# Performance work log

Hardware: AMD Instinct MI355X
Metric: run time of the kernel (lower is better)

The kernel has to match this reference:

```python
import jax, jax.numpy as jnp
import numpy as np

H = 1024      # hidden_size
NH = 16       # num_heads
HD = H // NH  # head_dim


def setup_inputs() -> dict:
    key = jax.random.key(0)
    k1, k2, k3 = jax.random.split(key, 3)
    x = jax.random.normal(k1, (2, 2048, H), dtype=jnp.float32)
    # torch Linear weights: [out, in]; init ~ small scale
    w_qkv = jax.random.normal(k2, (3 * H, H), dtype=jnp.float32) * (1.0 / np.sqrt(H))
    w_out = jax.random.normal(k3, (H, H), dtype=jnp.float32) * (1.0 / np.sqrt(H))
    return {"x": x, "w_qkv": w_qkv, "w_out": w_out}


def reference(x, w_qkv, w_out):
    B, S, _ = x.shape
    qkv = jnp.einsum("bsh,oh->bso", x, w_qkv)              # [B,S,3H]
    qkv = qkv.reshape(B, S, 3, NH, HD).transpose(2, 0, 3, 1, 4)  # [3,B,NH,S,HD]
    q, k, v = qkv[0], qkv[1], qkv[2]
    scale = 1.0 / np.sqrt(HD)
    scores = jnp.einsum("bhqd,bhkd->bhqk", q, k) * scale   # [B,NH,S,S]
    causal = jnp.tril(jnp.ones((S, S), dtype=bool))
    scores = jnp.where(causal, scores, jnp.finfo(scores.dtype).min)
    attn = jax.nn.softmax(scores, axis=-1)
    out = jnp.einsum("bhqk,bhkd->bhqd", attn, v)           # [B,NH,S,HD]
    out = out.transpose(0, 2, 1, 3).reshape(B, S, H)
    return jnp.einsum("bsh,oh->bso", out, w_out)
```

## Files before the change

kernel.cpp:

```cpp
#include <hip/hip_runtime.h>
#include <hip/hip_fp16.h>


typedef _Float16 half8 __attribute__((ext_vector_type(8)));
typedef _Float16 half4 __attribute__((ext_vector_type(4)));
typedef float f32x4 __attribute__((ext_vector_type(4)));

typedef const __attribute__((address_space(1))) void gvoid_t;
typedef __attribute__((address_space(3))) void lvoid_t;

#define LOG2E 1.4426950408889634f
#define QSCALE (0.125f * LOG2E)

__global__ void cast_all_f16(const float* __restrict__ x, const float* __restrict__ wq,
                             const float* __restrict__ wo, _Float16* __restrict__ xh,
                             _Float16* __restrict__ wqh, _Float16* __restrict__ woh) {
  int i = blockIdx.x * blockDim.x + threadIdx.x;
  const float* src;
  _Float16* dst;
  int off;
  if (i < 524288) { src = x; dst = xh; off = i; }
  else if (i < 917504) { src = wq; dst = wqh; off = i - 524288; }
  else { src = wo; dst = woh; off = i - 917504; }
  const float4* p = reinterpret_cast<const float4*>(src) + (size_t)off * 2;
  float4 a = p[0], b = p[1];
  half8 h;
  h[0] = (_Float16)a.x; h[1] = (_Float16)a.y; h[2] = (_Float16)a.z; h[3] = (_Float16)a.w;
  h[4] = (_Float16)b.x; h[5] = (_Float16)b.y; h[6] = (_Float16)b.z; h[7] = (_Float16)b.w;
  reinterpret_cast<half8*>(dst)[off] = h;
}

__global__ __launch_bounds__(256) void gemm_qkv(
    const _Float16* __restrict__ A, const _Float16* __restrict__ B,
    _Float16* __restrict__ Qo, _Float16* __restrict__ Ko, _Float16* __restrict__ Vto)
{
  __shared__ __align__(16) _Float16 As[128 * 32];
  __shared__ __align__(16) _Float16 Bs[128 * 32];
  const int tid = threadIdx.x;
  const int lane = tid & 63;
  const int w = tid >> 6;
  const int lr = lane & 15, hi = lane >> 4;
  const int wr = w >> 1, wc = w & 1;
  const int gm = blockIdx.y, gn = blockIdx.x;
  const _Float16* gA = A + (size_t)gm * 128 * 1024;
  const _Float16* gB = B + (size_t)gn * 128 * 1024;
  f32x4 acc[4][4] = {};

#define STAGE2(gp, sp)                                                                  \
  { _Pragma("unroll") for (int i_ = 0; i_ < 2; ++i_) {                                  \
      int c_ = i_ * 256 + tid; int r_ = c_ >> 2; int ko_ = (c_ & 3) * 8;                \
      __builtin_amdgcn_global_load_lds((gvoid_t*)((gp) + r_ * 1024 + ko_),              \
                                       (lvoid_t*)((sp) + c_ * 8), 16, 0, 0);            \
    } }

  STAGE2(gA, As)
  STAGE2(gB, Bs)
  for (int ks = 0;; ++ks) {
    __syncthreads();
    half8 af[4], bf[4];
#pragma unroll
    for (int mi = 0; mi < 4; ++mi)
      af[mi] = *reinterpret_cast<const half8*>(As + (wr * 64 + mi * 16 + lr) * 32 + hi * 8);
#pragma unroll
    for (int ni = 0; ni < 4; ++ni)
      bf[ni] = *reinterpret_cast<const half8*>(Bs + (wc * 64 + ni * 16 + lr) * 32 + hi * 8);
#pragma unroll
    for (int mi = 0; mi < 4; ++mi)
#pragma unroll
      for (int ni = 0; ni < 4; ++ni)
        acc[mi][ni] = __builtin_amdgcn_mfma_f32_16x16x32_f16(af[mi], bf[ni], acc[mi][ni], 0, 0, 0);
    if (ks == 31) break;
    __syncthreads();
    STAGE2(gA + (ks + 1) * 32, As)
    STAGE2(gB + (ks + 1) * 32, Bs)
  }

  const int row0 = gm * 128 + wr * 64;
  const int col0 = gn * 128 + wc * 64;
#pragma unroll
  for (int ni = 0; ni < 4; ++ni) {
    int col = col0 + ni * 16 + lr;
    int t = col >> 10, h = (col >> 6) & 15, d = col & 63;
#pragma unroll
    for (int mi = 0; mi < 4; ++mi) {
      int row = row0 + mi * 16 + hi * 4;
      int b = row >> 11, s = row & 2047;
      if (t == 2) {
        half4 pk = { (_Float16)acc[mi][ni][0], (_Float16)acc[mi][ni][1],
                     (_Float16)acc[mi][ni][2], (_Float16)acc[mi][ni][3] };
        *reinterpret_cast<half4*>(Vto + ((size_t)(b * 16 + h) * 64 + d) * 2048 + s) = pk;
      } else if (t == 0) {
#pragma unroll
        for (int j = 0; j < 4; ++j)
          Qo[(size_t)((b * 16 + h) * 2048 + s + j) * 64 + d] =
              (_Float16)(acc[mi][ni][j] * QSCALE);
      } else {
#pragma unroll
        for (int j = 0; j < 4; ++j)
          Ko[(size_t)((b * 16 + h) * 2048 + s + j) * 64 + d] = (_Float16)acc[mi][ni][j];
      }
    }
  }
}

__global__ __launch_bounds__(256) void gemm_out64(
    const _Float16* __restrict__ A, const _Float16* __restrict__ B,
    float* __restrict__ Co)
{
  __shared__ __align__(16) _Float16 As[64 * 32];
  __shared__ __align__(16) _Float16 Bs[128 * 32];
  const int tid = threadIdx.x;
  const int lane = tid & 63;
  const int w = tid >> 6;
  const int lr = lane & 15, hi = lane >> 4;
  const int gm = blockIdx.y, gn = blockIdx.x;
  const _Float16* gA = A + (size_t)gm * 64 * 1024;
  const _Float16* gB = B + (size_t)gn * 128 * 1024;
  f32x4 acc[4][2] = {};

#define STAGEA(gp)                                                                      \
  { int r_ = tid >> 2; int ko_ = (tid & 3) * 8;                                         \
    __builtin_amdgcn_global_load_lds((gvoid_t*)((gp) + r_ * 1024 + ko_),                \
                                     (lvoid_t*)(As + tid * 8), 16, 0, 0); }

  STAGEA(gA)
  STAGE2(gB, Bs)
  for (int ks = 0;; ++ks) {
    __syncthreads();
    half8 af[4], bf[2];
#pragma unroll
    for (int mi = 0; mi < 4; ++mi)
      af[mi] = *reinterpret_cast<const half8*>(As + (mi * 16 + lr) * 32 + hi * 8);
#pragma unroll
    for (int ni = 0; ni < 2; ++ni)
      bf[ni] = *reinterpret_cast<const half8*>(Bs + (w * 32 + ni * 16 + lr) * 32 + hi * 8);
#pragma unroll
    for (int mi = 0; mi < 4; ++mi)
#pragma unroll
      for (int ni = 0; ni < 2; ++ni)
        acc[mi][ni] = __builtin_amdgcn_mfma_f32_16x16x32_f16(af[mi], bf[ni], acc[mi][ni], 0, 0, 0);
    if (ks == 31) break;
    __syncthreads();
    STAGEA(gA + (ks + 1) * 32)
    STAGE2(gB + (ks + 1) * 32, Bs)
  }
#undef STAGEA
#undef STAGE2

#pragma unroll
  for (int mi = 0; mi < 4; ++mi)
#pragma unroll
    for (int j = 0; j < 4; ++j) {
      int row = gm * 64 + mi * 16 + hi * 4 + j;
#pragma unroll
      for (int ni = 0; ni < 2; ++ni) {
        int col = gn * 128 + w * 32 + ni * 16 + lr;
        Co[(size_t)row * 1024 + col] = acc[mi][ni][j];
      }
    }
}

__global__ __launch_bounds__(256, 2) void attn_f16(
    const _Float16* __restrict__ Qg, const _Float16* __restrict__ Kg,
    const _Float16* __restrict__ Vtg, _Float16* __restrict__ AO)
{
  const int bid = blockIdx.x;
  const int virt = ((bid & 7) << 6) | (bid >> 3);
  const int p = virt & 15;
  const int bh = virt >> 4;
  const int tid = threadIdx.x;
  const int w = tid >> 6, lane = tid & 63;
  const int lr = lane & 15, hi = lane >> 4;
  const _Float16* Qh = Qg + (size_t)bh * 2048 * 64;
  const _Float16* Kh = Kg + (size_t)bh * 2048 * 64;
  const _Float16* Vh = Vtg + (size_t)bh * 64 * 2048;
  const int b = bh >> 4, h = bh & 15;

  __shared__ __align__(16) _Float16 Kst[2][64 * 64];
  __shared__ __align__(16) _Float16 Vst[2][64 * 64];
  __shared__ __align__(16) _Float16 Plds[4][16][88];
  _Float16(*P)[88] = Plds[w];

  auto STAGE = [&](int buf, int kt) {
    const int k0 = kt * 64;
#pragma unroll
    for (int i = 0; i < 2; ++i) {
      int f = i * 256 + tid, r = f >> 3, s = f & 7, ss = s ^ (r & 7);
      __builtin_amdgcn_global_load_lds((gvoid_t*)(Kh + (size_t)(k0 + r) * 64 + ss * 8),
                                       (lvoid_t*)(&Kst[buf][f * 8]), 16, 0, 0);
    }
#pragma unroll
    for (int i = 0; i < 2; ++i) {
      int f = i * 256 + tid, r = f >> 3, s = f & 7, ss = s ^ (r & 7);
      __builtin_amdgcn_global_load_lds((gvoid_t*)(Vh + (size_t)r * 2048 + k0 + ss * 8),
                                       (lvoid_t*)(&Vst[buf][f * 8]), 16, 0, 0);
    }
  };

  auto PHASE = [&](int q0, int nkt) {
    const int qg0 = q0 + w * 16;
    half8 qf[2];
#pragma unroll
    for (int kk = 0; kk < 2; ++kk)
      qf[kk] = *reinterpret_cast<const half8*>(Qh + (size_t)(qg0 + lr) * 64 + kk * 32 + hi * 8);
    f32x4 accO[4] = {};
    f32x4 mrun, lrun;
#pragma unroll
    for (int j = 0; j < 4; ++j) { mrun[j] = -1e30f; lrun[j] = 0.f; }

    asm volatile("s_barrier" ::: "memory");
    STAGE(0, 0);
    for (int kt = 0; kt < nkt; ++kt) {
      const int k0 = kt * 64;
      const int cur = kt & 1;
      if (kt + 1 < nkt) {
        STAGE(cur ^ 1, kt + 1);
        asm volatile("s_waitcnt vmcnt(4)" ::: "memory");
      } else {
        asm volatile("s_waitcnt vmcnt(0)" ::: "memory");
      }
      __builtin_amdgcn_sched_barrier(0);
      asm volatile("s_barrier" ::: "memory");
      half8 kf[4][2], vf[2][4];
#pragma unroll
      for (int ni = 0; ni < 4; ++ni)
#pragma unroll
        for (int kk = 0; kk < 2; ++kk)
          kf[ni][kk] = *reinterpret_cast<const half8*>(
              &Kst[cur][(ni * 16 + lr) * 64 + ((kk * 4 + hi) ^ (lr & 7)) * 8]);
#pragma unroll
      for (int kk = 0; kk < 2; ++kk)
#pragma unroll
        for (int nd = 0; nd < 4; ++nd)
          vf[kk][nd] = *reinterpret_cast<const half8*>(
              &Vst[cur][(nd * 16 + lr) * 64 + ((kk * 4 + hi) ^ (lr & 7)) * 8]);
      f32x4 accS[4] = {};
#pragma unroll
      for (int ni = 0; ni < 4; ++ni)
#pragma unroll
        for (int kk = 0; kk < 2; ++kk)
          accS[ni] = __builtin_amdgcn_mfma_f32_16x16x32_f16(qf[kk], kf[ni][kk], accS[ni], 0, 0, 0);
      if (kt == nkt - 1) {
#pragma unroll
        for (int ni = 0; ni < 4; ++ni)
#pragma unroll
          for (int j = 0; j < 4; ++j) {
            int colg = k0 + ni * 16 + lr;
            int rowg = qg0 + hi * 4 + j;
            if (colg > rowg) accS[ni][j] = -1e30f;
          }
      }
      f32x4 rmax = accS[0];
#pragma unroll
      for (int ni = 1; ni < 4; ++ni)
#pragma unroll
        for (int j = 0; j < 4; ++j) rmax[j] = fmaxf(rmax[j], accS[ni][j]);
#pragma unroll
      for (int d = 1; d < 16; d <<= 1)
#pragma unroll
        for (int j = 0; j < 4; ++j) rmax[j] = fmaxf(rmax[j], __shfl_xor(rmax[j], d));
      f32x4 mnew, corr;
#pragma unroll
      for (int j = 0; j < 4; ++j) {
        mnew[j] = fmaxf(mrun[j], rmax[j]);
        corr[j] = exp2f(mrun[j] - mnew[j]);
        mrun[j] = mnew[j];
      }
      f32x4 rsum = {};
#pragma unroll
      for (int ni = 0; ni < 4; ++ni)
#pragma unroll
        for (int j = 0; j < 4; ++j) {
          float pv = exp2f(accS[ni][j] - mnew[j]);
          rsum[j] += pv;
          P[hi * 4 + j][ni * 16 + lr] = (_Float16)pv;
        }
#pragma unroll
      for (int d = 1; d < 16; d <<= 1)
#pragma unroll
        for (int j = 0; j < 4; ++j) rsum[j] += __shfl_xor(rsum[j], d);
#pragma unroll
      for (int j = 0; j < 4; ++j) lrun[j] = lrun[j] * corr[j] + rsum[j];
#pragma unroll
      for (int nd = 0; nd < 4; ++nd)
#pragma unroll
        for (int j = 0; j < 4; ++j) accO[nd][j] *= corr[j];
#pragma unroll
      for (int kk = 0; kk < 2; ++kk) {
        half8 pa = *reinterpret_cast<const half8*>(&P[lr][kk * 32 + hi * 8]);
#pragma unroll
        for (int nd = 0; nd < 4; ++nd)
          accO[nd] = __builtin_amdgcn_mfma_f32_16x16x32_f16(pa, vf[kk][nd], accO[nd], 0, 0, 0);
      }
      asm volatile("s_barrier" ::: "memory");
    }
    f32x4 inv;
#pragma unroll
    for (int j = 0; j < 4; ++j) inv[j] = 1.0f / lrun[j];
#pragma unroll
    for (int nd = 0; nd < 4; ++nd)
#pragma unroll
      for (int j = 0; j < 4; ++j) {
        int s = qg0 + hi * 4 + j;
        int d = nd * 16 + lr;
        AO[(size_t)(b * 2048 + s) * 1024 + h * 64 + d] = (_Float16)(accO[nd][j] * inv[j]);
      }
  };

  PHASE(p * 64, p + 1);
  PHASE((31 - p) * 64, 32 - p);
}

extern "C" void kernel_launch(void* const* d_in, const int* in_sizes, int n_in,
                              void* d_out, int out_size, void* d_ws, size_t ws_size,
                              hipStream_t stream) {
  const float* x = (const float*)d_in[0];
  const float* wqkv = (const float*)d_in[1];
  const float* wout = (const float*)d_in[2];
  float* out = (float*)d_out;
  char* ws = (char*)d_ws;
  _Float16* xh  = (_Float16*)(ws + (size_t)0);
  _Float16* wqh = (_Float16*)(ws + ((size_t)8 << 20));
  _Float16* woh = (_Float16*)(ws + ((size_t)14 << 20));
  _Float16* Qb  = (_Float16*)(ws + ((size_t)16 << 20));
  _Float16* Kb  = (_Float16*)(ws + ((size_t)24 << 20));
  _Float16* Vtb = (_Float16*)(ws + ((size_t)32 << 20));
  _Float16* AOb = (_Float16*)(ws + ((size_t)40 << 20));

  cast_all_f16<<<dim3(4096), 256, 0, stream>>>(x, wqkv, wout, xh, wqh, woh);
  gemm_qkv<<<dim3(24, 32), 256, 0, stream>>>(xh, wqh, Qb, Kb, Vtb);
  attn_f16<<<dim3(512), 256, 0, stream>>>(Qb, Kb, Vtb, AOb);
  gemm_out64<<<dim3(8, 64), 256, 0, stream>>>(AOb, woh, out);
}
```

Before: 205.1 us.

## Transpose attention MFMA operands so softmax rows reduce per lane

Swaps the MFMA A/B operands for the QK^T and PV products, so each lane holds one query row (indexed by lr) across its accumulator values. Row max and row sum then need two cross-lane shuffles instead of four, the running max and sum become scalars, P is written to LDS and the output to global memory as packed half4 vectors, and the P buffer stride shrinks to 72. s_setprio is also raised around the MFMA blocks. The aim is less VALU, shuffle and scattered-store overhead in the softmax. The risk is that the new LDS stride causes bank conflicts and that the causal mask indexing in the transposed layout is wrong.

```diff
diff --git a/kernel.cpp b/kernel.cpp
--- a/kernel.cpp
+++ b/kernel.cpp
@@ -178,8 +178,8 @@
 
   __shared__ __align__(16) _Float16 Kst[2][64 * 64];
   __shared__ __align__(16) _Float16 Vst[2][64 * 64];
-  __shared__ __align__(16) _Float16 Plds[4][16][88];
-  _Float16(*P)[88] = Plds[w];
+  __shared__ __align__(16) _Float16 Plds[4][16][72];
+  _Float16(*P)[72] = Plds[w];
 
   auto STAGE = [&](int buf, int kt) {
     const int k0 = kt * 64;
@@ -204,9 +204,7 @@
     for (int kk = 0; kk < 2; ++kk)
       qf[kk] = *reinterpret_cast<const half8*>(Qh + (size_t)(qg0 + lr) * 64 + kk * 32 + hi * 8);
     f32x4 accO[4] = {};
-    f32x4 mrun, lrun;
-#pragma unroll
-    for (int j = 0; j < 4; ++j) { mrun[j] = -1e30f; lrun[j] = 0.f; }
+    float mrun = -1e30f, lrun = 0.f;
 
     asm volatile("s_barrier" ::: "memory");
     STAGE(0, 0);
@@ -235,76 +233,76 @@
           vf[kk][nd] = *reinterpret_cast<const half8*>(
               &Vst[cur][(nd * 16 + lr) * 64 + ((kk * 4 + hi) ^ (lr & 7)) * 8]);
       f32x4 accS[4] = {};
+      __builtin_amdgcn_s_setprio(1);
 #pragma unroll
       for (int ni = 0; ni < 4; ++ni)
 #pragma unroll
         for (int kk = 0; kk < 2; ++kk)
-          accS[ni] = __builtin_amdgcn_mfma_f32_16x16x32_f16(qf[kk], kf[ni][kk], accS[ni], 0, 0, 0);
+          accS[ni] = __builtin_amdgcn_mfma_f32_16x16x32_f16(kf[ni][kk], qf[kk], accS[ni], 0, 0, 0);
+      __builtin_amdgcn_s_setprio(0);
       if (kt == nkt - 1) {
+        const int rowg = qg0 + lr;
 #pragma unroll
         for (int ni = 0; ni < 4; ++ni)
 #pragma unroll
           for (int j = 0; j < 4; ++j) {
-            int colg = k0 + ni * 16 + lr;
-            int rowg = qg0 + hi * 4 + j;
-            if (colg > rowg) accS[ni][j] = -1e30f;
+            int keyg = k0 + ni * 16 + hi * 4 + j;
+            if (keyg > rowg) accS[ni][j] = -1e30f;
           }
       }
-      f32x4 rmax = accS[0];
+      f32x4 m4 = accS[0];
 #pragma unroll
       for (int ni = 1; ni < 4; ++ni)
 #pragma unroll
-        for (int j = 0; j < 4; ++j) rmax[j] = fmaxf(rmax[j], accS[ni][j]);
-#pragma unroll
-      for (int d = 1; d < 16; d <<= 1)
-#pragma unroll
-        for (int j = 0; j < 4; ++j) rmax[j] = fmaxf(rmax[j], __shfl_xor(rmax[j], d));
-      f32x4 mnew, corr;
-#pragma unroll
-      for (int j = 0; j < 4; ++j) {
-        mnew[j] = fmaxf(mrun[j], rmax[j]);
-        corr[j] = exp2f(mrun[j] - mnew[j]);
-        mrun[j] = mnew[j];
-      }
-      f32x4 rsum = {};
+        for (int j = 0; j < 4; ++j) m4[j] = fmaxf(m4[j], accS[ni][j]);
+      float rm = fmaxf(fmaxf(m4[0], m4[1]), fmaxf(m4[2], m4[3]));
+      rm = fmaxf(rm, __shfl_xor(rm, 16));
+      rm = fmaxf(rm, __shfl_xor(rm, 32));
+      const float mnew = fmaxf(mrun, rm);
+      const float corr = exp2f(mrun - mnew);
+      mrun = mnew;
 #pragma unroll
       for (int ni = 0; ni < 4; ++ni)
 #pragma unroll
-        for (int j = 0; j < 4; ++j) {
-          float pv = exp2f(accS[ni][j] - mnew[j]);
-          rsum[j] += pv;
-          P[hi * 4 + j][ni * 16 + lr] = (_Float16)pv;
-        }
-#pragma unroll
-      for (int d = 1; d < 16; d <<= 1)
-#pragma unroll
-        for (int j = 0; j < 4; ++j) rsum[j] += __shfl_xor(rsum[j], d);
-#pragma unroll
-      for (int j = 0; j < 4; ++j) lrun[j] = lrun[j] * corr[j] + rsum[j];
+        for (int j = 0; j < 4; ++j) accS[ni][j] = exp2f(accS[ni][j] - mnew);
+      f32x4 s4 = accS[0];
+#pragma unroll
+      for (int ni = 1; ni < 4; ++ni)
+#pragma unroll
+        for (int j = 0; j < 4; ++j) s4[j] += accS[ni][j];
+      float rs = (s4[0] + s4[1]) + (s4[2] + s4[3]);
+      rs += __shfl_xor(rs, 16);
+      rs += __shfl_xor(rs, 32);
+      lrun = lrun * corr + rs;
 #pragma unroll
       for (int nd = 0; nd < 4; ++nd)
 #pragma unroll
-        for (int j = 0; j < 4; ++j) accO[nd][j] *= corr[j];
+        for (int j = 0; j < 4; ++j) accO[nd][j] *= corr;
+#pragma unroll
+      for (int ni = 0; ni < 4; ++ni) {
+        half4 pk = { (_Float16)accS[ni][0], (_Float16)accS[ni][1],
+                     (_Float16)accS[ni][2], (_Float16)accS[ni][3] };
+        *reinterpret_cast<half4*>(&P[lr][ni * 16 + hi * 4]) = pk;
+      }
+      __builtin_amdgcn_s_setprio(1);
 #pragma unroll
       for (int kk = 0; kk < 2; ++kk) {
-        half8 pa = *reinterpret_cast<const half8*>(&P[lr][kk * 32 + hi * 8]);
+        half8 pb = *reinterpret_cast<const half8*>(&P[lr][kk * 32 + hi * 8]);
 #pragma unroll
         for (int nd = 0; nd < 4; ++nd)
-          accO[nd] = __builtin_amdgcn_mfma_f32_16x16x32_f16(pa, vf[kk][nd], accO[nd], 0, 0, 0);
-      }
+          accO[nd] = __builtin_amdgcn_mfma_f32_16x16x32_f16(vf[kk][nd], pb, accO[nd], 0, 0, 0);
+      }
+      __builtin_amdgcn_s_setprio(0);
       asm volatile("s_barrier" ::: "memory");
     }
-    f32x4 inv;
-#pragma unroll
-    for (int j = 0; j < 4; ++j) inv[j] = 1.0f / lrun[j];
-#pragma unroll
-    for (int nd = 0; nd < 4; ++nd)
-#pragma unroll
-      for (int j = 0; j < 4; ++j) {
-        int s = qg0 + hi * 4 + j;
-        int d = nd * 16 + lr;
-        AO[(size_t)(b * 2048 + s) * 1024 + h * 64 + d] = (_Float16)(accO[nd][j] * inv[j]);
-      }
+    const float inv = 1.0f / lrun;
+    const size_t base = (size_t)(b * 2048 + qg0 + lr) * 1024 + h * 64;
+#pragma unroll
+    for (int nd = 0; nd < 4; ++nd) {
+      half4 ov = { (_Float16)(accO[nd][0] * inv), (_Float16)(accO[nd][1] * inv),
+                   (_Float16)(accO[nd][2] * inv), (_Float16)(accO[nd][3] * inv) };
+      *reinterpret_cast<half4*>(AO + base + nd * 16 + hi * 4) = ov;
+    }
   };
 
   PHASE(p * 64, p + 1);
```

Result: faster. 184.7 us (-10.0%).
